# Performance work log

Measured on AMD Instinct MI355X. Metric: run time of the kernel, lower is better.

The kernel has to match this reference:

```python
import jax, jax.numpy as jnp
import numpy as np

N = 50000        # nodes
E = 500000       # edges
NUM = 4          # sampled intermediate neighbors per edge (self.num)
F = 64           # in_feats == out_feats (transform=False)
D = 32           # dist_dim
NB = 64          # embedding rows = len(boundaries)+1


def setup_inputs() -> dict:
    key = jax.random.key(0)
    ks = jax.random.split(key, 10)
    feat = jax.random.normal(ks[0], (N, F), jnp.float32)
    loc = jax.random.uniform(ks[1], (N, 3), jnp.float32)          # 3D positions in unit cube
    boundaries = jnp.sort(jax.random.uniform(ks[2], (NB - 1,), jnp.float32, 0.0, 2.0))
    embed_table = jax.random.normal(ks[3], (NB, D), jnp.float32)
    G_w = jax.random.normal(ks[4], (F, D), jnp.float32) / np.sqrt(D)      # Linear(dist_dim->out, no bias)
    agg_w = jax.random.normal(ks[5], (F, 2 * F), jnp.float32) / np.sqrt(2 * F)  # Linear(2*out->out)
    agg_b = jnp.zeros((F,), jnp.float32)
    src = jax.random.randint(ks[6], (E,), 0, N, jnp.int32)
    dst = jax.random.randint(ks[7], (E,), 0, N, jnp.int32)
    inter_ids = jax.random.randint(ks[8], (E, NUM), 0, N, jnp.int32)
    return dict(feat=feat, loc=loc, boundaries=boundaries, embed_table=embed_table,
                G_w=G_w, agg_w=agg_w, agg_b=agg_b, src=src, dst=dst, inter_ids=inter_ids)


def reference(feat, loc, boundaries, embed_table, G_w, agg_w, agg_b, src, dst, inter_ids):
    n = feat.shape[0]
    ones = jnp.ones((src.shape[0],), feat.dtype)
    # symmetric-ish degree normalization: d0 = in_deg^-0.5, d2 = out_deg^-0.5
    in_deg = jax.ops.segment_sum(ones, dst, num_segments=n)
    out_deg = jax.ops.segment_sum(ones, src, num_segments=n)
    d0 = jnp.clip(in_deg, 1.0) ** -0.5   # [N]
    d2 = jnp.clip(out_deg, 1.0) ** -0.5  # [N]

    # dist1 = ||loc[dst] - loc[src]||_2, bucketize -> embed -> G
    dist1 = jnp.linalg.norm(loc[dst] - loc[src], axis=1)              # [E]
    de1 = embed_table[jnp.searchsorted(boundaries, dist1)] @ G_w.T    # [E, F]

    # intermediate sampled neighbors: dist to each sampled node from edge src
    pos_src = loc[src]                                                # [E, 3]
    inter_pos = loc[inter_ids]                                        # [E, NUM, 3]
    dist_ = jnp.linalg.norm(pos_src[:, None, :] - inter_pos, axis=-1) # [E, NUM]
    de_ = embed_table[jnp.searchsorted(boundaries, dist_)] @ G_w.T    # [E, NUM, F]
    inter_h = feat[inter_ids]                                         # [E, NUM, F]
    dist_embed_dot_h = (de_ * inter_h).mean(axis=1)                   # [E, F]

    # h = d0[dst] * d2[src] * agg_fc([de1 * h_src, dist_embed_dot_h])
    cat = jnp.concatenate([de1 * feat[src], dist_embed_dot_h], axis=1)  # [E, 2F]
    msg = (d0[dst] * d2[src])[:, None] * (cat @ agg_w.T + agg_b)        # [E, F]

    # update_all(copy_e('h'), sum) -> scatter-sum messages to dst
    ft = jax.ops.segment_sum(msg, dst, num_segments=n)                  # [N, F]
    return ft
```

## Files before the change

kernel.cpp:

```cpp
#include <hip/hip_runtime.h>
#include <math.h>

#define LUTN 1024
#define LUTSCALE 512.0f


__global__ __launch_bounds__(256) void prep_kernel(
    const float* __restrict__ embed, const float* __restrict__ G_w,
    const float* __restrict__ boundaries, const float* __restrict__ feat,
    const float* __restrict__ loc,
    float* __restrict__ M, int* __restrict__ lut,
    int* __restrict__ d2i, int* __restrict__ cnt,
    unsigned short* __restrict__ featH, float4* __restrict__ loc4, int N) {

    const int gid = blockIdx.x * 256 + threadIdx.x;
    const int gsz = gridDim.x * 256;
    for (int i = gid; i < N; i += gsz) { cnt[i] = 0; d2i[i] = 0; }
    for (int i = gid; i < 4096; i += gsz) {
        int b = i >> 6, f = i & 63;
        float acc = 0.f;
        #pragma unroll
        for (int dd = 0; dd < 32; ++dd) acc += embed[b * 32 + dd] * G_w[f * 32 + dd];
        M[i] = acc;
    }
    for (int i = gid; i < LUTN; i += gsz) {
        float left = (float)i * (1.0f / LUTSCALE);
        int c = 0;
        for (int j = 0; j < 63; ++j) c += (boundaries[j] < left) ? 1 : 0;
        lut[i] = c;
    }
    const int nq = N * 16;
    for (int i = gid; i < nq; i += gsz) {
        float4 v = ((const float4*)feat)[i];
        unsigned ux = __float_as_uint(v.x), uy = __float_as_uint(v.y);
        unsigned uz = __float_as_uint(v.z), uw = __float_as_uint(v.w);
        ushort4 h;
        h.x = (unsigned short)((ux + 0x7FFFu + ((ux >> 16) & 1u)) >> 16);
        h.y = (unsigned short)((uy + 0x7FFFu + ((uy >> 16) & 1u)) >> 16);
        h.z = (unsigned short)((uz + 0x7FFFu + ((uz >> 16) & 1u)) >> 16);
        h.w = (unsigned short)((uw + 0x7FFFu + ((uw >> 16) & 1u)) >> 16);
        ((ushort4*)featH)[i] = h;
    }
    for (int i = gid; i < N; i += gsz)
        loc4[i] = make_float4(loc[3 * i], loc[3 * i + 1], loc[3 * i + 2], 0.f);
}


__global__ __launch_bounds__(256) void edge_kernel(
    const float4* __restrict__ loc4, const float* __restrict__ boundaries,
    const int* __restrict__ lut,
    const int* __restrict__ src, const int* __restrict__ dst,
    const int* __restrict__ inter,
    int* __restrict__ cnt, int* __restrict__ d2i,
    int4* __restrict__ recE, int E) {

    __shared__ int lut_s[LUTN];
    __shared__ float bl[64];
    ((int4*)lut_s)[threadIdx.x] = ((const int4*)lut)[threadIdx.x];
    if (threadIdx.x < 64)
        bl[threadIdx.x] = (threadIdx.x < 63) ? boundaries[threadIdx.x] : 3.4e38f;
    __syncthreads();

    const int e = blockIdx.x * 256 + threadIdx.x;
    if (e >= E) return;

    const int s = src[e], d = dst[e];
    const int4 ii = ((const int4*)inter)[e];

    const float4 ps = loc4[s];
    float dist[5];
    {
        float4 pd = loc4[d];
        float dx = pd.x - ps.x, dy = pd.y - ps.y, dz = pd.z - ps.z;
        dist[0] = sqrtf(dx * dx + dy * dy + dz * dz);
    }
    const int id4[4] = {ii.x, ii.y, ii.z, ii.w};
    #pragma unroll
    for (int j = 0; j < 4; ++j) {
        float4 pt = loc4[id4[j]];
        float dx = pt.x - ps.x, dy = pt.y - ps.y, dz = pt.z - ps.z;
        dist[1 + j] = sqrtf(dx * dx + dy * dy + dz * dz);
    }
    unsigned pack = 0;
    #pragma unroll
    for (int q = 0; q < 5; ++q) {
        float dq = dist[q];
        int cell = (int)(dq * LUTSCALE);
        cell = (cell > LUTN - 1) ? (LUTN - 1) : cell;
        int b = lut_s[cell];
        while (b < 63 && bl[b] < dq) ++b;
        while (b > 0 && bl[b - 1] >= dq) --b;
        pack |= ((unsigned)b) << (6 * q);
    }

    const int r = atomicAdd(&cnt[d], 1);
    atomicAdd(&d2i[s], 1);

    recE[e] = make_int4(s | (ii.x << 16), ii.y | (ii.z << 16), ii.w | (r << 16), (int)pack);
}


__global__ __launch_bounds__(1024) void scan_block_kernel(
    const int* __restrict__ cnt, int* __restrict__ startv,
    int* __restrict__ part, int N) {

    __shared__ int wsum[16];
    const int t = threadIdx.x, lane = t & 63, wv = t >> 6;
    const int i = blockIdx.x * 1024 + t;

    int v = (i < N) ? cnt[i] : 0;
    int x = v;
    #pragma unroll
    for (int off = 1; off < 64; off <<= 1) { int y = __shfl_up(x, off); if (lane >= off) x += y; }
    if (lane == 63) wsum[wv] = x;
    __syncthreads();
    if (t < 16) {
        int w = wsum[t], xx = w;
        #pragma unroll
        for (int off = 1; off < 16; off <<= 1) { int y = __shfl_up(xx, off); if (t >= off) xx += y; }
        wsum[t] = xx - w;
    }
    __syncthreads();
    int incl = x + wsum[wv];
    if (i < N) startv[i] = incl - v;
    if (t == 1023) part[blockIdx.x] = incl;
}

__device__ __forceinline__ void load_chunkoff(const int* __restrict__ part, int nb,
                                              int* __restrict__ co) {
    if (threadIdx.x < 64) {
        int v = (threadIdx.x < nb) ? part[threadIdx.x] : 0;
        int x = v;
        #pragma unroll
        for (int off = 1; off < 64; off <<= 1) {
            int y = __shfl_up(x, off);
            if ((threadIdx.x & 63) >= off) x += y;
        }
        co[threadIdx.x] = x - v;
    }
    __syncthreads();
}


__global__ __launch_bounds__(256) void scatter_kernel(
    const int4* __restrict__ recE, const int* __restrict__ dst,
    const int* __restrict__ startv, const int* __restrict__ part,
    const int* __restrict__ d2i, int4* __restrict__ rec, int E, int nb) {

    __shared__ int co[64];
    load_chunkoff(part, nb, co);

    const int e = blockIdx.x * 256 + threadIdx.x;
    if (e >= E) return;
    const int4 a = recE[e];
    const int s = a.x & 0xFFFF;
    const int r = ((unsigned)a.z) >> 16;
    const int d = dst[e];
    const int pos = startv[d] + co[d >> 10] + r;
    const float w = rsqrtf(fmaxf((float)d2i[s], 1.0f));
    unsigned uw = __float_as_uint(w);
    unsigned wb = (uw + 0x7FFFu + ((uw >> 16) & 1u)) & 0xFFFF0000u;
    rec[pos] = make_int4(a.x, a.y, (a.z & 0xFFFF) | (int)wb, a.w);
}


__global__ __launch_bounds__(256) void node_kernel(
    const unsigned short* __restrict__ featH, const float* __restrict__ M,
    const int* __restrict__ cnt, const int* __restrict__ startv,
    const int* __restrict__ part, const int4* __restrict__ rec,
    float* __restrict__ cat, float* __restrict__ swb, int N, int nb) {

    __shared__ float Ms[4096];
    __shared__ int co[64];
    #pragma unroll
    for (int i = 0; i < 4; ++i)
        ((float4*)Ms)[threadIdx.x + 256 * i] = ((const float4*)M)[threadIdx.x + 256 * i];
    load_chunkoff(part, nb, co);

    const int lane = threadIdx.x & 63;
    const int wid  = threadIdx.x >> 6;
    const int d    = blockIdx.x * 4 + wid;
    if (d >= N) return;

    const int deg  = __builtin_amdgcn_readfirstlane(cnt[d]);
    const int base = __builtin_amdgcn_readfirstlane(startv[d] + co[d >> 10]);
    const int4* rp = rec + base;

    float acc0 = 0.f, acc1 = 0.f, sw = 0.f;

    #pragma unroll 4
    for (int k = 0; k < deg; ++k) {
        const int4 r = rp[k];
        const int s  = r.x & 0xFFFF;
        const int i0 = ((unsigned)r.x) >> 16;
        const int i1 = r.y & 0xFFFF;
        const int i2 = ((unsigned)r.y) >> 16;
        const int i3 = r.z & 0xFFFF;
        const float w = __uint_as_float((unsigned)r.z & 0xFFFF0000u);
        const unsigned pk = (unsigned)r.w;

        const float fs = __uint_as_float(((unsigned)featH[(size_t)s  * 64 + lane]) << 16);
        const float f0 = __uint_as_float(((unsigned)featH[(size_t)i0 * 64 + lane]) << 16);
        const float f1 = __uint_as_float(((unsigned)featH[(size_t)i1 * 64 + lane]) << 16);
        const float f2 = __uint_as_float(((unsigned)featH[(size_t)i2 * 64 + lane]) << 16);
        const float f3 = __uint_as_float(((unsigned)featH[(size_t)i3 * 64 + lane]) << 16);
        const float m0 = Ms[(pk & 63u) * 64 + lane];
        const float m1 = Ms[((pk >> 6) & 63u) * 64 + lane];
        const float m2 = Ms[((pk >> 12) & 63u) * 64 + lane];
        const float m3 = Ms[((pk >> 18) & 63u) * 64 + lane];
        const float m4 = Ms[((pk >> 24) & 63u) * 64 + lane];

        acc0 = fmaf(m0 * fs, w, acc0);
        float t = m1 * f0 + m2 * f1 + m3 * f2 + m4 * f3;
        acc1 = fmaf(0.25f * t, w, acc1);
        sw += w;
    }

    cat[(size_t)d * 128 + lane]      = acc0;
    cat[(size_t)d * 128 + 64 + lane] = acc1;
    if (lane == 0) swb[d] = sw;
}


__global__ __launch_bounds__(256) void epilogue_kernel(
    const float* __restrict__ cat, const float* __restrict__ agg_w,
    const float* __restrict__ agg_b, const float* __restrict__ swb,
    const int* __restrict__ cnt, float* __restrict__ out, int N) {

    const int lane = threadIdx.x & 63;
    const int wid  = threadIdx.x >> 6;

    float4 aw[32];
    const float4* awp = (const float4*)(agg_w + (size_t)lane * 128);
    #pragma unroll
    for (int i = 0; i < 32; ++i) aw[i] = awp[i];
    const float bias = agg_b[lane];

    const int gw = blockIdx.x * 4 + wid;
    const int stride = gridDim.x * 4;

    for (int d0i = gw; d0i < N; d0i += stride) {
        const int du = __builtin_amdgcn_readfirstlane(d0i);
        const float* cp = cat + (size_t)du * 128;
        float a0 = bias * swb[du], a1 = 0.f, a2 = 0.f, a3 = 0.f;
        #pragma unroll
        for (int k4 = 0; k4 < 32; k4 += 4) {
            float4 c0 = ((const float4*)cp)[k4];
            float4 c1 = ((const float4*)cp)[k4 + 1];
            float4 c2 = ((const float4*)cp)[k4 + 2];
            float4 c3 = ((const float4*)cp)[k4 + 3];
            a0 = fmaf(aw[k4].x, c0.x, a0); a0 = fmaf(aw[k4].y, c0.y, a0);
            a0 = fmaf(aw[k4].z, c0.z, a0); a0 = fmaf(aw[k4].w, c0.w, a0);
            a1 = fmaf(aw[k4+1].x, c1.x, a1); a1 = fmaf(aw[k4+1].y, c1.y, a1);
            a1 = fmaf(aw[k4+1].z, c1.z, a1); a1 = fmaf(aw[k4+1].w, c1.w, a1);
            a2 = fmaf(aw[k4+2].x, c2.x, a2); a2 = fmaf(aw[k4+2].y, c2.y, a2);
            a2 = fmaf(aw[k4+2].z, c2.z, a2); a2 = fmaf(aw[k4+2].w, c2.w, a2);
            a3 = fmaf(aw[k4+3].x, c3.x, a3); a3 = fmaf(aw[k4+3].y, c3.y, a3);
            a3 = fmaf(aw[k4+3].z, c3.z, a3); a3 = fmaf(aw[k4+3].w, c3.w, a3);
        }
        const float d0v = rsqrtf(fmaxf((float)cnt[du], 1.0f));
        out[(size_t)du * 64 + lane] = d0v * ((a0 + a1) + (a2 + a3));
    }
}


extern "C" void kernel_launch(void* const* d_in, const int* in_sizes, int n_in,
                              void* d_out, int out_size, void* d_ws, size_t ws_size,
                              hipStream_t stream) {
    const float* feat       = (const float*)d_in[0];
    const float* loc        = (const float*)d_in[1];
    const float* boundaries = (const float*)d_in[2];
    const float* embed      = (const float*)d_in[3];
    const float* G_w        = (const float*)d_in[4];
    const float* agg_w      = (const float*)d_in[5];
    const float* agg_b      = (const float*)d_in[6];
    const int*   src        = (const int*)d_in[7];
    const int*   dst        = (const int*)d_in[8];
    const int*   inter      = (const int*)d_in[9];

    const int N = in_sizes[0] / 64;
    const int E = in_sizes[7];

    char* w = (char*)d_ws;
    auto take = [&](size_t bytes) { char* p = w; w += (bytes + 15) & ~(size_t)15; return p; };
    float*          M      = (float*)take(4096 * 4);
    int*            lut    = (int*)  take(LUTN * 4);
    int*            d2i    = (int*)  take((size_t)N * 4);
    int*            cnt    = (int*)  take((size_t)N * 4);
    int*            startv = (int*)  take((size_t)N * 4);
    int*            part   = (int*)  take(64 * 4);
    int4*           recE   = (int4*) take((size_t)E * 16);
    int4*           rec    = (int4*) take((size_t)E * 16);
    float*          cat    = (float*)take((size_t)N * 128 * 4);
    float*          swb    = (float*)take((size_t)N * 4);
    unsigned short* featH  = (unsigned short*)take((size_t)N * 64 * 2);
    float4*         loc4   = (float4*)take((size_t)N * 16);
    float*          out    = (float*)d_out;

    const int eb = (E + 255) / 256;
    const int nb = (N + 1023) / 1024;

    prep_kernel<<<1024, 256, 0, stream>>>(embed, G_w, boundaries, feat, loc,
                                          M, lut, d2i, cnt, featH, loc4, N);
    edge_kernel<<<eb, 256, 0, stream>>>(loc4, boundaries, lut, src, dst, inter,
                                        cnt, d2i, recE, E);
    scan_block_kernel<<<nb, 1024, 0, stream>>>(cnt, startv, part, N);
    scatter_kernel<<<eb, 256, 0, stream>>>(recE, dst, startv, part, d2i, rec, E, nb);
    node_kernel<<<(N + 3) / 4, 256, 0, stream>>>(featH, M, cnt, startv, part, rec,
                                                 cat, swb, N, nb);
    epilogue_kernel<<<768, 256, 0, stream>>>(cat, agg_w, agg_b, swb, cnt, out, N);
}
```

Baseline: 233.4 us.

## Fuse prep into edge kernel and epilogue GEMV into node kernel

Removes the separate prep kernel by having each edge block build its bucket LUT in shared memory, read loc directly instead of a padded float4 copy, and do the feature bf16 conversion and M/WtT precompute in a grid-stride tail. The epilogue kernel is dropped: each node wave stages its 128-wide concat vector in LDS and applies the transposed agg_w directly, so the N×128 cat buffer no longer round-trips through global memory. The zeroing of the counters moves to a memset. In exchange, every edge block recomputes the LUT, loc reads become unaligned scalar loads, and the node kernel takes on extra per-node GEMV work.

```diff
diff --git a/kernel.cpp b/kernel.cpp
--- a/kernel.cpp
+++ b/kernel.cpp
@@ -5,30 +5,72 @@
 #define LUTSCALE 512.0f
 
 
-__global__ __launch_bounds__(256) void prep_kernel(
-    const float* __restrict__ embed, const float* __restrict__ G_w,
-    const float* __restrict__ boundaries, const float* __restrict__ feat,
-    const float* __restrict__ loc,
-    float* __restrict__ M, int* __restrict__ lut,
-    int* __restrict__ d2i, int* __restrict__ cnt,
-    unsigned short* __restrict__ featH, float4* __restrict__ loc4, int N) {
+__global__ __launch_bounds__(256) void edge_kernel(
+    const float* __restrict__ loc, const float* __restrict__ boundaries,
+    const int* __restrict__ src, const int* __restrict__ dst,
+    const int* __restrict__ inter,
+    int* __restrict__ cnt, int* __restrict__ d2i, int4* __restrict__ recE,
+    const float* __restrict__ feat, const float* __restrict__ embed,
+    const float* __restrict__ G_w, const float* __restrict__ agg_w,
+    unsigned short* __restrict__ featH, float* __restrict__ M,
+    float* __restrict__ WtT, int E, int N) {
+
+    __shared__ int lut_s[LUTN];
+    __shared__ float bl[64];
+
+    if (threadIdx.x < 64)
+        bl[threadIdx.x] = (threadIdx.x < 63) ? boundaries[threadIdx.x] : 3.4e38f;
+    __syncthreads();
+    #pragma unroll
+    for (int q = 0; q < LUTN / 256; ++q) {
+        int i = threadIdx.x + q * 256;
+        float left = (float)i * (1.0f / LUTSCALE);
+        int c = 0;
+        #pragma unroll
+        for (int j = 0; j < 63; ++j) c += (bl[j] < left) ? 1 : 0;
+        lut_s[i] = c;
+    }
+    __syncthreads();
+
+    const int e = blockIdx.x * 256 + threadIdx.x;
+    if (e < E) {
+        const int s = src[e], d = dst[e];
+        const int4 ii = ((const int4*)inter)[e];
+
+        const float sx = loc[3 * s], sy = loc[3 * s + 1], sz = loc[3 * s + 2];
+        float dist[5];
+        {
+            float dx = loc[3 * d] - sx, dy = loc[3 * d + 1] - sy, dz = loc[3 * d + 2] - sz;
+            dist[0] = sqrtf(dx * dx + dy * dy + dz * dz);
+        }
+        const int id4[4] = {ii.x, ii.y, ii.z, ii.w};
+        #pragma unroll
+        for (int j = 0; j < 4; ++j) {
+            int t = id4[j];
+            float dx = loc[3 * t] - sx, dy = loc[3 * t + 1] - sy, dz = loc[3 * t + 2] - sz;
+            dist[1 + j] = sqrtf(dx * dx + dy * dy + dz * dz);
+        }
+        unsigned pack = 0;
+        #pragma unroll
+        for (int q = 0; q < 5; ++q) {
+            float dq = dist[q];
+            int cell = (int)(dq * LUTSCALE);
+            cell = (cell > LUTN - 1) ? (LUTN - 1) : cell;
+            int b = lut_s[cell];
+            while (b < 63 && bl[b] < dq) ++b;
+            while (b > 0 && bl[b - 1] >= dq) --b;
+            pack |= ((unsigned)b) << (6 * q);
+        }
+
+        const int r = atomicAdd(&cnt[d], 1);
+        atomicAdd(&d2i[s], 1);
+
+        recE[e] = make_int4(s | (ii.x << 16), ii.y | (ii.z << 16), ii.w | (r << 16), (int)pack);
+    }
 
     const int gid = blockIdx.x * 256 + threadIdx.x;
     const int gsz = gridDim.x * 256;
-    for (int i = gid; i < N; i += gsz) { cnt[i] = 0; d2i[i] = 0; }
-    for (int i = gid; i < 4096; i += gsz) {
-        int b = i >> 6, f = i & 63;
-        float acc = 0.f;
-        #pragma unroll
-        for (int dd = 0; dd < 32; ++dd) acc += embed[b * 32 + dd] * G_w[f * 32 + dd];
-        M[i] = acc;
-    }
-    for (int i = gid; i < LUTN; i += gsz) {
-        float left = (float)i * (1.0f / LUTSCALE);
-        int c = 0;
-        for (int j = 0; j < 63; ++j) c += (boundaries[j] < left) ? 1 : 0;
-        lut[i] = c;
-    }
+
     const int nq = N * 16;
     for (int i = gid; i < nq; i += gsz) {
         float4 v = ((const float4*)feat)[i];
@@ -41,62 +83,17 @@
         h.w = (unsigned short)((uw + 0x7FFFu + ((uw >> 16) & 1u)) >> 16);
         ((ushort4*)featH)[i] = h;
     }
-    for (int i = gid; i < N; i += gsz)
-        loc4[i] = make_float4(loc[3 * i], loc[3 * i + 1], loc[3 * i + 2], 0.f);
-}
-
-
-__global__ __launch_bounds__(256) void edge_kernel(
-    const float4* __restrict__ loc4, const float* __restrict__ boundaries,
-    const int* __restrict__ lut,
-    const int* __restrict__ src, const int* __restrict__ dst,
-    const int* __restrict__ inter,
-    int* __restrict__ cnt, int* __restrict__ d2i,
-    int4* __restrict__ recE, int E) {
-
-    __shared__ int lut_s[LUTN];
-    __shared__ float bl[64];
-    ((int4*)lut_s)[threadIdx.x] = ((const int4*)lut)[threadIdx.x];
-    if (threadIdx.x < 64)
-        bl[threadIdx.x] = (threadIdx.x < 63) ? boundaries[threadIdx.x] : 3.4e38f;
-    __syncthreads();
-
-    const int e = blockIdx.x * 256 + threadIdx.x;
-    if (e >= E) return;
-
-    const int s = src[e], d = dst[e];
-    const int4 ii = ((const int4*)inter)[e];
-
-    const float4 ps = loc4[s];
-    float dist[5];
-    {
-        float4 pd = loc4[d];
-        float dx = pd.x - ps.x, dy = pd.y - ps.y, dz = pd.z - ps.z;
-        dist[0] = sqrtf(dx * dx + dy * dy + dz * dz);
-    }
-    const int id4[4] = {ii.x, ii.y, ii.z, ii.w};
-    #pragma unroll
-    for (int j = 0; j < 4; ++j) {
-        float4 pt = loc4[id4[j]];
-        float dx = pt.x - ps.x, dy = pt.y - ps.y, dz = pt.z - ps.z;
-        dist[1 + j] = sqrtf(dx * dx + dy * dy + dz * dz);
-    }
-    unsigned pack = 0;
-    #pragma unroll
-    for (int q = 0; q < 5; ++q) {
-        float dq = dist[q];
-        int cell = (int)(dq * LUTSCALE);
-        cell = (cell > LUTN - 1) ? (LUTN - 1) : cell;
-        int b = lut_s[cell];
-        while (b < 63 && bl[b] < dq) ++b;
-        while (b > 0 && bl[b - 1] >= dq) --b;
-        pack |= ((unsigned)b) << (6 * q);
-    }
-
-    const int r = atomicAdd(&cnt[d], 1);
-    atomicAdd(&d2i[s], 1);
-
-    recE[e] = make_int4(s | (ii.x << 16), ii.y | (ii.z << 16), ii.w | (r << 16), (int)pack);
+    for (int i = gid; i < 4096; i += gsz) {
+        int b = i >> 6, f = i & 63;
+        float acc = 0.f;
+        #pragma unroll
+        for (int dd = 0; dd < 32; ++dd) acc += embed[b * 32 + dd] * G_w[f * 32 + dd];
+        M[i] = acc;
+    }
+    for (int i = gid; i < 8192; i += gsz) {
+        int k = i >> 6, f = i & 63;
+        WtT[i] = agg_w[f * 128 + k];
+    }
 }
 
 
@@ -166,11 +163,13 @@
 
 __global__ __launch_bounds__(256) void node_kernel(
     const unsigned short* __restrict__ featH, const float* __restrict__ M,
+    const float* __restrict__ WtT, const float* __restrict__ agg_b,
     const int* __restrict__ cnt, const int* __restrict__ startv,
     const int* __restrict__ part, const int4* __restrict__ rec,
-    float* __restrict__ cat, float* __restrict__ swb, int N, int nb) {
+    float* __restrict__ out, int N, int nb) {
 
     __shared__ float Ms[4096];
+    __shared__ float cs[4][128];
     __shared__ int co[64];
     #pragma unroll
     for (int i = 0; i < 4; ++i)
@@ -182,6 +181,7 @@
     const int d    = blockIdx.x * 4 + wid;
     if (d >= N) return;
 
+    const float bias = agg_b[lane];
     const int deg  = __builtin_amdgcn_readfirstlane(cnt[d]);
     const int base = __builtin_amdgcn_readfirstlane(startv[d] + co[d >> 10]);
     const int4* rp = rec + base;
@@ -216,51 +216,21 @@
         sw += w;
     }
 
-    cat[(size_t)d * 128 + lane]      = acc0;
-    cat[(size_t)d * 128 + 64 + lane] = acc1;
-    if (lane == 0) swb[d] = sw;
-}
-
-
-__global__ __launch_bounds__(256) void epilogue_kernel(
-    const float* __restrict__ cat, const float* __restrict__ agg_w,
-    const float* __restrict__ agg_b, const float* __restrict__ swb,
-    const int* __restrict__ cnt, float* __restrict__ out, int N) {
-
-    const int lane = threadIdx.x & 63;
-    const int wid  = threadIdx.x >> 6;
-
-    float4 aw[32];
-    const float4* awp = (const float4*)(agg_w + (size_t)lane * 128);
-    #pragma unroll
-    for (int i = 0; i < 32; ++i) aw[i] = awp[i];
-    const float bias = agg_b[lane];
-
-    const int gw = blockIdx.x * 4 + wid;
-    const int stride = gridDim.x * 4;
-
-    for (int d0i = gw; d0i < N; d0i += stride) {
-        const int du = __builtin_amdgcn_readfirstlane(d0i);
-        const float* cp = cat + (size_t)du * 128;
-        float a0 = bias * swb[du], a1 = 0.f, a2 = 0.f, a3 = 0.f;
-        #pragma unroll
-        for (int k4 = 0; k4 < 32; k4 += 4) {
-            float4 c0 = ((const float4*)cp)[k4];
-            float4 c1 = ((const float4*)cp)[k4 + 1];
-            float4 c2 = ((const float4*)cp)[k4 + 2];
-            float4 c3 = ((const float4*)cp)[k4 + 3];
-            a0 = fmaf(aw[k4].x, c0.x, a0); a0 = fmaf(aw[k4].y, c0.y, a0);
-            a0 = fmaf(aw[k4].z, c0.z, a0); a0 = fmaf(aw[k4].w, c0.w, a0);
-            a1 = fmaf(aw[k4+1].x, c1.x, a1); a1 = fmaf(aw[k4+1].y, c1.y, a1);
-            a1 = fmaf(aw[k4+1].z, c1.z, a1); a1 = fmaf(aw[k4+1].w, c1.w, a1);
-            a2 = fmaf(aw[k4+2].x, c2.x, a2); a2 = fmaf(aw[k4+2].y, c2.y, a2);
-            a2 = fmaf(aw[k4+2].z, c2.z, a2); a2 = fmaf(aw[k4+2].w, c2.w, a2);
-            a3 = fmaf(aw[k4+3].x, c3.x, a3); a3 = fmaf(aw[k4+3].y, c3.y, a3);
-            a3 = fmaf(aw[k4+3].z, c3.z, a3); a3 = fmaf(aw[k4+3].w, c3.w, a3);
-        }
-        const float d0v = rsqrtf(fmaxf((float)cnt[du], 1.0f));
-        out[(size_t)du * 64 + lane] = d0v * ((a0 + a1) + (a2 + a3));
-    }
+    cs[wid][lane]      = acc0;
+    cs[wid][64 + lane] = acc1;
+
+    float a0 = bias * sw, a1 = 0.f, a2 = 0.f, a3 = 0.f;
+    #pragma unroll 8
+    for (int k = 0; k < 128; k += 4) {
+        float c0 = cs[wid][k], c1 = cs[wid][k + 1];
+        float c2 = cs[wid][k + 2], c3 = cs[wid][k + 3];
+        a0 = fmaf(WtT[(k + 0) * 64 + lane], c0, a0);
+        a1 = fmaf(WtT[(k + 1) * 64 + lane], c1, a1);
+        a2 = fmaf(WtT[(k + 2) * 64 + lane], c2, a2);
+        a3 = fmaf(WtT[(k + 3) * 64 + lane], c3, a3);
+    }
+    const float d0v = rsqrtf(fmaxf((float)deg, 1.0f));
+    out[(size_t)d * 64 + lane] = d0v * ((a0 + a1) + (a2 + a3));
 }
 
 
@@ -284,29 +254,27 @@
     char* w = (char*)d_ws;
     auto take = [&](size_t bytes) { char* p = w; w += (bytes + 15) & ~(size_t)15; return p; };
     float*          M      = (float*)take(4096 * 4);
-    int*            lut    = (int*)  take(LUTN * 4);
+    float*          WtT    = (float*)take(8192 * 4);
     int*            d2i    = (int*)  take((size_t)N * 4);
     int*            cnt    = (int*)  take((size_t)N * 4);
     int*            startv = (int*)  take((size_t)N * 4);
     int*            part   = (int*)  take(64 * 4);
     int4*           recE   = (int4*) take((size_t)E * 16);
     int4*           rec    = (int4*) take((size_t)E * 16);
-    float*          cat    = (float*)take((size_t)N * 128 * 4);
-    float*          swb    = (float*)take((size_t)N * 4);
     unsigned short* featH  = (unsigned short*)take((size_t)N * 64 * 2);
-    float4*         loc4   = (float4*)take((size_t)N * 16);
     float*          out    = (float*)d_out;
 
     const int eb = (E + 255) / 256;
     const int nb = (N + 1023) / 1024;
 
-    prep_kernel<<<1024, 256, 0, stream>>>(embed, G_w, boundaries, feat, loc,
-                                          M, lut, d2i, cnt, featH, loc4, N);
-    edge_kernel<<<eb, 256, 0, stream>>>(loc4, boundaries, lut, src, dst, inter,
-                                        cnt, d2i, recE, E);
+    hipMemsetAsync(d2i, 0, (size_t)2 * N * sizeof(int), stream);
+
+    edge_kernel<<<eb, 256, 0, stream>>>(loc, boundaries, src, dst, inter,
+                                        cnt, d2i, recE,
+                                        feat, embed, G_w, agg_w,
+                                        featH, M, WtT, E, N);
     scan_block_kernel<<<nb, 1024, 0, stream>>>(cnt, startv, part, N);
     scatter_kernel<<<eb, 256, 0, stream>>>(recE, dst, startv, part, d2i, rec, E, nb);
-    node_kernel<<<(N + 3) / 4, 256, 0, stream>>>(featH, M, cnt, startv, part, rec,
-                                                 cat, swb, N, nb);
-    epilogue_kernel<<<768, 256, 0, stream>>>(cat, agg_w, agg_b, swb, cnt, out, N);
-}
+    node_kernel<<<(N + 3) / 4, 256, 0, stream>>>(featH, M, WtT, agg_b,
+                                                 cnt, startv, part, rec, out, N, nb);
+}
```

Result: slower. 249.0 us (+6.7%).

## Fuse prep work into edge kernel and zero counters with memset

Applied to the files above, without the earlier changes.

Removes the separate prep kernel. Each edge block now builds the bucket LUT in shared memory from the boundaries, and the same launch also runs the feat-to-bf16 conversion and the embed×G_w product in grid-stride loops. The edge pass reads the raw 3-float loc directly instead of a padded float4 copy, and cnt/d2i are cleared with a single memset that relies on the two arrays sitting next to each other in the workspace. This saves a kernel launch and the loc4/lut round trips, at the cost of every block recomputing the LUT and less aligned loc gathers.

```diff
diff --git a/kernel.cpp b/kernel.cpp
--- a/kernel.cpp
+++ b/kernel.cpp
@@ -5,30 +5,71 @@
 #define LUTSCALE 512.0f
 
 
-__global__ __launch_bounds__(256) void prep_kernel(
-    const float* __restrict__ embed, const float* __restrict__ G_w,
-    const float* __restrict__ boundaries, const float* __restrict__ feat,
-    const float* __restrict__ loc,
-    float* __restrict__ M, int* __restrict__ lut,
-    int* __restrict__ d2i, int* __restrict__ cnt,
-    unsigned short* __restrict__ featH, float4* __restrict__ loc4, int N) {
+__global__ __launch_bounds__(256) void edge_kernel(
+    const float* __restrict__ loc, const float* __restrict__ boundaries,
+    const int* __restrict__ src, const int* __restrict__ dst,
+    const int* __restrict__ inter,
+    int* __restrict__ cnt, int* __restrict__ d2i, int4* __restrict__ recE,
+    const float* __restrict__ feat, const float* __restrict__ embed,
+    const float* __restrict__ G_w,
+    unsigned short* __restrict__ featH, float* __restrict__ M, int E, int N) {
+
+    __shared__ int lut_s[LUTN];
+    __shared__ float bl[64];
+
+    if (threadIdx.x < 64)
+        bl[threadIdx.x] = (threadIdx.x < 63) ? boundaries[threadIdx.x] : 3.4e38f;
+    __syncthreads();
+    #pragma unroll
+    for (int q = 0; q < LUTN / 256; ++q) {
+        int i = threadIdx.x + q * 256;
+        float left = (float)i * (1.0f / LUTSCALE);
+        int c = 0;
+        #pragma unroll
+        for (int j = 0; j < 63; ++j) c += (bl[j] < left) ? 1 : 0;
+        lut_s[i] = c;
+    }
+    __syncthreads();
+
+    const int e = blockIdx.x * 256 + threadIdx.x;
+    if (e < E) {
+        const int s = src[e], d = dst[e];
+        const int4 ii = ((const int4*)inter)[e];
+
+        const float sx = loc[3 * s], sy = loc[3 * s + 1], sz = loc[3 * s + 2];
+        float dist[5];
+        {
+            float dx = loc[3 * d] - sx, dy = loc[3 * d + 1] - sy, dz = loc[3 * d + 2] - sz;
+            dist[0] = sqrtf(dx * dx + dy * dy + dz * dz);
+        }
+        const int id4[4] = {ii.x, ii.y, ii.z, ii.w};
+        #pragma unroll
+        for (int j = 0; j < 4; ++j) {
+            int t = id4[j];
+            float dx = loc[3 * t] - sx, dy = loc[3 * t + 1] - sy, dz = loc[3 * t + 2] - sz;
+            dist[1 + j] = sqrtf(dx * dx + dy * dy + dz * dz);
+        }
+        unsigned pack = 0;
+        #pragma unroll
+        for (int q = 0; q < 5; ++q) {
+            float dq = dist[q];
+            int cell = (int)(dq * LUTSCALE);
+            cell = (cell > LUTN - 1) ? (LUTN - 1) : cell;
+            int b = lut_s[cell];
+            while (b < 63 && bl[b] < dq) ++b;
+            while (b > 0 && bl[b - 1] >= dq) --b;
+            pack |= ((unsigned)b) << (6 * q);
+        }
+
+        const int r = atomicAdd(&cnt[d], 1);
+        atomicAdd(&d2i[s], 1);
+
+        recE[e] = make_int4(s | (ii.x << 16), ii.y | (ii.z << 16), ii.w | (r << 16), (int)pack);
+    }
 
     const int gid = blockIdx.x * 256 + threadIdx.x;
     const int gsz = gridDim.x * 256;
-    for (int i = gid; i < N; i += gsz) { cnt[i] = 0; d2i[i] = 0; }
-    for (int i = gid; i < 4096; i += gsz) {
-        int b = i >> 6, f = i & 63;
-        float acc = 0.f;
-        #pragma unroll
-        for (int dd = 0; dd < 32; ++dd) acc += embed[b * 32 + dd] * G_w[f * 32 + dd];
-        M[i] = acc;
-    }
-    for (int i = gid; i < LUTN; i += gsz) {
-        float left = (float)i * (1.0f / LUTSCALE);
-        int c = 0;
-        for (int j = 0; j < 63; ++j) c += (boundaries[j] < left) ? 1 : 0;
-        lut[i] = c;
-    }
+
     const int nq = N * 16;
     for (int i = gid; i < nq; i += gsz) {
         float4 v = ((const float4*)feat)[i];
@@ -41,62 +82,13 @@
         h.w = (unsigned short)((uw + 0x7FFFu + ((uw >> 16) & 1u)) >> 16);
         ((ushort4*)featH)[i] = h;
     }
-    for (int i = gid; i < N; i += gsz)
-        loc4[i] = make_float4(loc[3 * i], loc[3 * i + 1], loc[3 * i + 2], 0.f);
-}
-
-
-__global__ __launch_bounds__(256) void edge_kernel(
-    const float4* __restrict__ loc4, const float* __restrict__ boundaries,
-    const int* __restrict__ lut,
-    const int* __restrict__ src, const int* __restrict__ dst,
-    const int* __restrict__ inter,
-    int* __restrict__ cnt, int* __restrict__ d2i,
-    int4* __restrict__ recE, int E) {
-
-    __shared__ int lut_s[LUTN];
-    __shared__ float bl[64];
-    ((int4*)lut_s)[threadIdx.x] = ((const int4*)lut)[threadIdx.x];
-    if (threadIdx.x < 64)
-        bl[threadIdx.x] = (threadIdx.x < 63) ? boundaries[threadIdx.x] : 3.4e38f;
-    __syncthreads();
-
-    const int e = blockIdx.x * 256 + threadIdx.x;
-    if (e >= E) return;
-
-    const int s = src[e], d = dst[e];
-    const int4 ii = ((const int4*)inter)[e];
-
-    const float4 ps = loc4[s];
-    float dist[5];
-    {
-        float4 pd = loc4[d];
-        float dx = pd.x - ps.x, dy = pd.y - ps.y, dz = pd.z - ps.z;
-        dist[0] = sqrtf(dx * dx + dy * dy + dz * dz);
-    }
-    const int id4[4] = {ii.x, ii.y, ii.z, ii.w};
-    #pragma unroll
-    for (int j = 0; j < 4; ++j) {
-        float4 pt = loc4[id4[j]];
-        float dx = pt.x - ps.x, dy = pt.y - ps.y, dz = pt.z - ps.z;
-        dist[1 + j] = sqrtf(dx * dx + dy * dy + dz * dz);
-    }
-    unsigned pack = 0;
-    #pragma unroll
-    for (int q = 0; q < 5; ++q) {
-        float dq = dist[q];
-        int cell = (int)(dq * LUTSCALE);
-        cell = (cell > LUTN - 1) ? (LUTN - 1) : cell;
-        int b = lut_s[cell];
-        while (b < 63 && bl[b] < dq) ++b;
-        while (b > 0 && bl[b - 1] >= dq) --b;
-        pack |= ((unsigned)b) << (6 * q);
-    }
-
-    const int r = atomicAdd(&cnt[d], 1);
-    atomicAdd(&d2i[s], 1);
-
-    recE[e] = make_int4(s | (ii.x << 16), ii.y | (ii.z << 16), ii.w | (r << 16), (int)pack);
+    for (int i = gid; i < 4096; i += gsz) {
+        int b = i >> 6, f = i & 63;
+        float acc = 0.f;
+        #pragma unroll
+        for (int dd = 0; dd < 32; ++dd) acc += embed[b * 32 + dd] * G_w[f * 32 + dd];
+        M[i] = acc;
+    }
 }
 
 
@@ -284,7 +276,6 @@
     char* w = (char*)d_ws;
     auto take = [&](size_t bytes) { char* p = w; w += (bytes + 15) & ~(size_t)15; return p; };
     float*          M      = (float*)take(4096 * 4);
-    int*            lut    = (int*)  take(LUTN * 4);
     int*            d2i    = (int*)  take((size_t)N * 4);
     int*            cnt    = (int*)  take((size_t)N * 4);
     int*            startv = (int*)  take((size_t)N * 4);
@@ -294,16 +285,16 @@
     float*          cat    = (float*)take((size_t)N * 128 * 4);
     float*          swb    = (float*)take((size_t)N * 4);
     unsigned short* featH  = (unsigned short*)take((size_t)N * 64 * 2);
-    float4*         loc4   = (float4*)take((size_t)N * 16);
     float*          out    = (float*)d_out;
 
     const int eb = (E + 255) / 256;
     const int nb = (N + 1023) / 1024;
 
-    prep_kernel<<<1024, 256, 0, stream>>>(embed, G_w, boundaries, feat, loc,
-                                          M, lut, d2i, cnt, featH, loc4, N);
-    edge_kernel<<<eb, 256, 0, stream>>>(loc4, boundaries, lut, src, dst, inter,
-                                        cnt, d2i, recE, E);
+    hipMemsetAsync(d2i, 0, (size_t)2 * N * sizeof(int), stream);
+
+    edge_kernel<<<eb, 256, 0, stream>>>(loc, boundaries, src, dst, inter,
+                                        cnt, d2i, recE,
+                                        feat, embed, G_w, featH, M, E, N);
     scan_block_kernel<<<nb, 1024, 0, stream>>>(cnt, startv, part, N);
     scatter_kernel<<<eb, 256, 0, stream>>>(recE, dst, startv, part, d2i, rec, E, nb);
     node_kernel<<<(N + 3) / 4, 256, 0, stream>>>(featH, M, cnt, startv, part, rec,
```

After: 240.9 us. 3.2% more time.
